# Kernel optimization log

Hardware: AMD Instinct MI355X
Metric: run time of the kernel (lower is better)

Reference implementation:

```python
import jax, jax.numpy as jnp
import numpy as np

B, T, E, H = 2, 2048, 1024, 16
D = E // H            # head dim = 64
ROT = D // 2          # rotary_dim = 32 (only first half of head dim is rotated)
THETA = 10000.0


def _rope(x):
    # x: (B, H, T, D). Faithful to rotary_embedding_torch.rotate_queries_or_keys
    # with dim=ROT: rotate first ROT features, interleaved-pair style, pass rest.
    t = x.shape[-2]
    inv = 1.0 / (THETA ** (jnp.arange(0, ROT, 2, dtype=jnp.float32) / ROT))   # (ROT//2,)
    freqs = jnp.arange(t, dtype=jnp.float32)[:, None] * inv[None, :]          # (T, ROT//2)
    freqs = jnp.repeat(freqs, 2, axis=-1)                                      # (T, ROT)
    cos, sin = jnp.cos(freqs), jnp.sin(freqs)
    xr, xp = x[..., :ROT], x[..., ROT:]
    p = xr.reshape(*xr.shape[:-1], ROT // 2, 2)
    rot = jnp.stack((-p[..., 1], p[..., 0]), axis=-1).reshape(xr.shape)
    return jnp.concatenate([xr * cos + rot * sin, xp], axis=-1)


def setup_inputs() -> dict:
    key = jax.random.key(0)
    k1, k2, k3 = jax.random.split(key, 3)
    query = jax.random.normal(k1, (B, T, E), dtype=jnp.float32)
    inputs = {
        "query": query,
        "key": query,            # ignored (cross_attention=False)
        "value": query,          # ignored
        "padding_mask": jnp.ones((B, T), dtype=bool),
        "in_proj_weight": jax.random.uniform(k2, (3 * E, E), dtype=jnp.float32),
        "out_proj_weight": jax.random.normal(k3, (E, E), dtype=jnp.float32) * (E ** -0.5),
    }
    return inputs


def reference(query, key, value, padding_mask, in_proj_weight, out_proj_weight):
    # cross_attention=False: key/value are overwritten by query
    key = query
    value = query
    q = query @ in_proj_weight[:E].T
    k = key @ in_proj_weight[E:2 * E].T
    v = value @ in_proj_weight[2 * E:].T
    # NOTE: raw reshape (B,T,E)->(B,H,T,D), exactly as in the torch module
    q = q.reshape(B, H, T, D)
    k = k.reshape(B, H, T, D)
    v = v.reshape(B, H, T, D)
    q = _rope(q)
    k = _rope(k)   # causal self-attention path: rotate keys too
    causal = jnp.tril(jnp.ones((T, T), dtype=bool))                 # (T, T)
    mask = causal[None, None] & padding_mask[:, None, None, :]      # (B,1,T,T) -> broadcast over H
    scores = jnp.einsum("bhqd,bhkd->bhqk", q, k) / jnp.sqrt(jnp.float32(D))
    scores = jnp.where(mask, scores, -jnp.inf)
    attn = jax.nn.softmax(scores, axis=-1)
    x = jnp.einsum("bhqk,bhkd->bhqd", attn, v)
    x = x.reshape(B, T, E)      # raw reshape back, as in torch
    return x @ out_proj_weight.T
```

## Files before the change

kernel.cpp:

```cpp
#include <hip/hip_runtime.h>
#include <stdint.h>

#define T_ 2048
#define E_ 1024

typedef __attribute__((ext_vector_type(8))) __bf16 bf16x8;
typedef __attribute__((ext_vector_type(4))) float f32x4;

__device__ __forceinline__ void gload_lds16(const void* g, void* l) {
  __builtin_amdgcn_global_load_lds(
      (const __attribute__((address_space(1))) unsigned int*)g,
      (__attribute__((address_space(3))) unsigned int*)l, 16, 0, 0);
}

__global__ __launch_bounds__(256) void k_split(const float4* __restrict__ src,
                                               ushort4* __restrict__ hi,
                                               ushort4* __restrict__ lo, int n4) {
  int i = blockIdx.x * 256 + threadIdx.x;
  if (i >= n4) return;
  float4 x = src[i];
  float xs[4] = {x.x, x.y, x.z, x.w};
  union { __bf16 b[4]; ushort4 u; } H, L;
#pragma unroll
  for (int j = 0; j < 4; ++j) {
    __bf16 h = (__bf16)xs[j];
    H.b[j] = h;
    L.b[j] = (__bf16)(xs[j] - (float)h);
  }
  hi[i] = H.u;
  lo[i] = L.u;
}

__global__ __launch_bounds__(256) void k_cvt(const float4* __restrict__ src,
                                             ushort4* __restrict__ dst, int n4) {
  int i = blockIdx.x * 256 + threadIdx.x;
  if (i >= n4) return;
  float4 x = src[i];
  float xs[4] = {x.x, x.y, x.z, x.w};
  union { __bf16 b[4]; ushort4 u; } H;
#pragma unroll
  for (int j = 0; j < 4; ++j) H.b[j] = (__bf16)xs[j];
  dst[i] = H.u;
}

__global__ __launch_bounds__(256) void k_table(float2* __restrict__ cs) {
  int i = blockIdx.x * 256 + threadIdx.x;
  int t = i >> 4, f = i & 15;
  double inv = pow(10000.0, -(double)f / 16.0);
  double ang = (double)t * inv;
  cs[i] = make_float2((float)cos(ang), (float)sin(ang));
}

template <int EPI, bool HILO>
__global__ __launch_bounds__(256) void k_gemm(const __bf16* __restrict__ Ah,
                                              const __bf16* __restrict__ Al,
                                              const __bf16* __restrict__ Bh,
                                              const __bf16* __restrict__ Bl,
                                              int M, int N, int K,
                                              const float2* __restrict__ cs,
                                              __bf16* __restrict__ qhi,
                                              __bf16* __restrict__ qlo,
                                              __bf16* __restrict__ khi,
                                              __bf16* __restrict__ klo,
                                              __bf16* __restrict__ v16,
                                              float* __restrict__ C32) {
  __shared__ __align__(16) __bf16 AsH[128 * 32];
  __shared__ __align__(16) __bf16 BsH[128 * 32];
  __shared__ __align__(16) __bf16 AsL[HILO ? 128 * 32 : 4];
  __shared__ __align__(16) __bf16 BsL[HILO ? 128 * 32 : 4];
  const int tid = threadIdx.x, lane = tid & 63, w = tid >> 6;
  const int wm = w >> 1, wn = w & 1;
  const int g = lane >> 4, d = lane & 15;
  const int m0 = blockIdx.y * 128, n0 = blockIdx.x * 128;

  f32x4 acc[4][4];
#pragma unroll
  for (int i = 0; i < 4; ++i)
#pragma unroll
    for (int j = 0; j < 4; ++j) acc[i][j] = (f32x4)(0.0f);

  const int row0 = tid >> 2, kc = tid & 3;
  const int row1 = 64 + row0;

  for (int k0 = 0; k0 < K; k0 += 32) {
    __syncthreads();
    gload_lds16(Ah + (size_t)(m0 + row0) * K + k0 + kc * 8, &AsH[w * 512]);
    gload_lds16(Ah + (size_t)(m0 + row1) * K + k0 + kc * 8, &AsH[2048 + w * 512]);
    gload_lds16(Bh + (size_t)(n0 + row0) * K + k0 + kc * 8, &BsH[w * 512]);
    gload_lds16(Bh + (size_t)(n0 + row1) * K + k0 + kc * 8, &BsH[2048 + w * 512]);
    if constexpr (HILO) {
      gload_lds16(Al + (size_t)(m0 + row0) * K + k0 + kc * 8, &AsL[w * 512]);
      gload_lds16(Al + (size_t)(m0 + row1) * K + k0 + kc * 8, &AsL[2048 + w * 512]);
      gload_lds16(Bl + (size_t)(n0 + row0) * K + k0 + kc * 8, &BsL[w * 512]);
      gload_lds16(Bl + (size_t)(n0 + row1) * K + k0 + kc * 8, &BsL[2048 + w * 512]);
    }
    __syncthreads();
    bf16x8 ah[4], bh[4], al[4], bl[4];
#pragma unroll
    for (int i = 0; i < 4; ++i) {
      ah[i] = *(const bf16x8*)&AsH[(wm * 64 + i * 16 + d) * 32 + g * 8];
      bh[i] = *(const bf16x8*)&BsH[(wn * 64 + i * 16 + d) * 32 + g * 8];
      if constexpr (HILO) {
        al[i] = *(const bf16x8*)&AsL[(wm * 64 + i * 16 + d) * 32 + g * 8];
        bl[i] = *(const bf16x8*)&BsL[(wn * 64 + i * 16 + d) * 32 + g * 8];
      }
    }
#pragma unroll
    for (int i = 0; i < 4; ++i)
#pragma unroll
      for (int j = 0; j < 4; ++j) {
        acc[i][j] = __builtin_amdgcn_mfma_f32_16x16x32_bf16(ah[i], bh[j], acc[i][j], 0, 0, 0);
        if constexpr (HILO) {
          acc[i][j] = __builtin_amdgcn_mfma_f32_16x16x32_bf16(al[i], bh[j], acc[i][j], 0, 0, 0);
          acc[i][j] = __builtin_amdgcn_mfma_f32_16x16x32_bf16(ah[i], bl[j], acc[i][j], 0, 0, 0);
        }
      }
  }

#pragma unroll
  for (int i = 0; i < 4; ++i) {
    const int rbase = m0 + wm * 64 + i * 16 + g * 4;
#pragma unroll
    for (int j = 0; j < 4; ++j) {
      const int col = n0 + wn * 64 + j * 16 + d;
#pragma unroll
      for (int r = 0; r < 4; ++r) {
        const float vv = acc[i][j][r];
        const int row = rbase + r;
        if constexpr (EPI == 0) {
          const float xp = __shfl_xor(vv, 1);
          const int which = col >> 10;
          const int cl = col & 1023;
          const int d2 = cl & 63;
          const int t2 = (row & 127) * 16 + (cl >> 6);
          float y;
          if (d2 < 32) {
            const float2 cse = cs[t2 * 16 + (d2 >> 1)];
            y = (d2 & 1) ? (vv * cse.x + xp * cse.y) : (vv * cse.x - xp * cse.y);
          } else {
            y = vv;
          }
          if (which == 0) y *= 0.18033688011112042f;
          const __bf16 hi = (__bf16)y;
          const __bf16 lo = (__bf16)(y - (float)hi);
          const size_t off = (size_t)row * 1024 + cl;
          (which ? khi : qhi)[off] = hi;
          (which ? klo : qlo)[off] = lo;
        } else if constexpr (EPI == 1) {
          C32[(size_t)row * N + col] = vv;
        } else {
          v16[(size_t)row * N + col] = (__bf16)vv;
        }
      }
    }
  }
}

__global__ __launch_bounds__(256) void k_vtrans(const __bf16* __restrict__ v16,
                                                __bf16* __restrict__ v16t) {
  __shared__ __bf16 TB[64][72];
  const int p = blockIdx.y, t0 = blockIdx.x * 64;
  const int tid = threadIdx.x;
  const int r = tid >> 2, c4 = (tid & 3) * 16;
  const __bf16* src = v16 + ((size_t)p * 2048 + t0 + r) * 64 + c4;
  bf16x8 A = *(const bf16x8*)src;
  bf16x8 B2 = *(const bf16x8*)(src + 8);
#pragma unroll
  for (int e = 0; e < 8; ++e) {
    TB[c4 + e][r] = A[e];
    TB[c4 + 8 + e][r] = B2[e];
  }
  __syncthreads();
  const int dd = tid >> 2, cc = (tid & 3) * 16;
  __bf16* dst = v16t + ((size_t)p * 64 + dd) * 2048 + t0 + cc;
  *(bf16x8*)dst = *(const bf16x8*)&TB[dd][cc];
  *(bf16x8*)(dst + 8) = *(const bf16x8*)&TB[dd][cc + 8];
}

__global__ __launch_bounds__(512, 4) void k_attn(const __bf16* __restrict__ qhi,
                                                 const __bf16* __restrict__ qlo,
                                                 const __bf16* __restrict__ khi,
                                                 const __bf16* __restrict__ klo,
                                                 const __bf16* __restrict__ v16t,
                                                 __bf16* __restrict__ x16,
                                                 float* __restrict__ po,
                                                 float* __restrict__ pm,
                                                 float* __restrict__ pl_) {
  __shared__ __align__(16) __bf16 KH[2][64 * 64];
  __shared__ __align__(16) __bf16 KL[2][64 * 64];
  __shared__ __align__(16) __bf16 VT[2][64 * 64];
  __shared__ __align__(16) __bf16 PL[8][16 * 72];

  const int b = blockIdx.x, panel = blockIdx.y;
  const int u0 = 9 * b;
  int qtA = 0;
  while (2 * (qtA + 1) * (qtA + 2) <= u0) ++qtA;
  const int cumA = 2 * qtA * (qtA + 1);
  const int cumB = 2 * (qtA + 1) * (qtA + 2);
  const int jloA = u0 - cumA;
  const bool two = (u0 + 9 > cumB);
  const int jhiA = two ? (cumB - 1 - cumA) : (u0 + 8 - cumA);
  const int jhiB = u0 + 8 - cumB;

  const int tid = threadIdx.x, lane = tid & 63, w = tid >> 6;
  const int g = lane >> 4, d = lane & 15;
  const size_t hb = (size_t)panel * T_ * 64;

  const int kr = tid >> 3, kc = tid & 7;
  const int swz = (kc ^ (kr & 7)) * 8;
  const __bf16* kB = khi + hb;
  const __bf16* lB = klo + hb;
  const __bf16* vB = v16t + (size_t)panel * (64 * T_);

#define STAGE(j, bb)                                                        \
  {                                                                         \
    gload_lds16(kB + (size_t)((j) * 64 + kr) * 64 + swz, &KH[bb][w * 512]); \
    gload_lds16(lB + (size_t)((j) * 64 + kr) * 64 + swz, &KL[bb][w * 512]); \
    gload_lds16(vB + (size_t)kr * T_ + (j) * 64 + swz, &VT[bb][w * 512]);   \
  }

  int cur = 0;
  STAGE(jloA, 0);

  for (int seg = 0; seg < 2; ++seg) {
    if (seg && !two) break;
    const int qt = qtA + seg;
    const int jlo = seg ? 0 : jloA;
    const int jhi = seg ? jhiB : jhiA;
    const int q0 = qt << 8;

    bf16x8 qh[2][2], ql[2][2];
#pragma unroll
    for (int rb = 0; rb < 2; ++rb) {
      const int rbi = w * 2 + rb;
      const size_t qrow = hb + (size_t)(q0 + rbi * 16 + d) * 64;
      qh[rb][0] = *(const bf16x8*)&qhi[qrow + g * 8];
      qh[rb][1] = *(const bf16x8*)&qhi[qrow + 32 + g * 8];
      ql[rb][0] = *(const bf16x8*)&qlo[qrow + g * 8];
      ql[rb][1] = *(const bf16x8*)&qlo[qrow + 32 + g * 8];
    }

    f32x4 o[2][4];
#pragma unroll
    for (int rb = 0; rb < 2; ++rb)
#pragma unroll
      for (int i = 0; i < 4; ++i) o[rb][i] = (f32x4)(0.0f);
    float m_[2] = {-__builtin_inff(), -__builtin_inff()};
    float l_[2] = {0.0f, 0.0f};

    for (int j = jlo; j <= jhi; ++j) {
      __syncthreads();
      if (j < jhi) {
        STAGE(j + 1, cur ^ 1);
      } else if (!seg && two) {
        STAGE(0, cur ^ 1);
      }

#pragma unroll
      for (int rb = 0; rb < 2; ++rb) {
        const int rbi = w * 2 + rb;
        const int qrow0 = q0 + rbi * 16;
        if (j * 64 > qrow0 + 15) continue;

        f32x4 s[4];
        __builtin_amdgcn_s_setprio(1);
#pragma unroll
        for (int f = 0; f < 4; ++f) {
          f32x4 accs = (f32x4)(0.0f);
          const int colr = f * 16 + d;
#pragma unroll
          for (int ds = 0; ds < 2; ++ds) {
            const int slot = ((ds * 4 + g) ^ (colr & 7)) * 8;
            const bf16x8 kf = *(const bf16x8*)&KH[cur][colr * 64 + slot];
            const bf16x8 lf = *(const bf16x8*)&KL[cur][colr * 64 + slot];
            accs = __builtin_amdgcn_mfma_f32_16x16x32_bf16(kf, qh[rb][ds], accs, 0, 0, 0);
            accs = __builtin_amdgcn_mfma_f32_16x16x32_bf16(kf, ql[rb][ds], accs, 0, 0, 0);
            accs = __builtin_amdgcn_mfma_f32_16x16x32_bf16(lf, qh[rb][ds], accs, 0, 0, 0);
          }
          s[f] = accs;
        }
        __builtin_amdgcn_s_setprio(0);

        if (j * 64 + 63 > qrow0) {
          const int qq = qrow0 + d;
#pragma unroll
          for (int f = 0; f < 4; ++f)
#pragma unroll
            for (int r = 0; r < 4; ++r) {
              const int kv = j * 64 + f * 16 + g * 4 + r;
              if (kv > qq) s[f][r] = -30000.0f;
            }
        }

        float pmax = fmaxf(fmaxf(s[0][0], s[0][1]), fmaxf(s[0][2], s[0][3]));
#pragma unroll
        for (int f = 1; f < 4; ++f)
          pmax = fmaxf(pmax, fmaxf(fmaxf(s[f][0], s[f][1]), fmaxf(s[f][2], s[f][3])));
        pmax = fmaxf(pmax, __shfl_xor(pmax, 16));
        pmax = fmaxf(pmax, __shfl_xor(pmax, 32));

        if (!__all(pmax - m_[rb] <= 11.5f)) {
          const float mnew = fmaxf(m_[rb], pmax);
          const float fac = exp2f(m_[rb] - mnew);
          m_[rb] = mnew;
          float facr[4];
#pragma unroll
          for (int r = 0; r < 4; ++r)
            facr[r] = __shfl(fac, (lane & 48) | (g * 4 + r));
#pragma unroll
          for (int ni = 0; ni < 4; ++ni)
#pragma unroll
            for (int r = 0; r < 4; ++r) o[rb][ni][r] *= facr[r];
          l_[rb] *= fac;
        }

        float sum = 0.0f;
#pragma unroll
        for (int f = 0; f < 4; ++f) {
          union { __bf16 b[4]; ushort4 u4; } pk;
#pragma unroll
          for (int r = 0; r < 4; ++r) {
            const float pv = exp2f(s[f][r] - m_[rb]);
            sum += pv;
            pk.b[r] = (__bf16)pv;
          }
          *(ushort4*)&PL[w][d * 72 + f * 16 + g * 4] = pk.u4;
        }
        sum += __shfl_xor(sum, 16);
        sum += __shfl_xor(sum, 32);
        l_[rb] += sum;

        __builtin_amdgcn_s_setprio(1);
#pragma unroll
        for (int ks = 0; ks < 2; ++ks) {
          const bf16x8 pa = *(const bf16x8*)&PL[w][d * 72 + ks * 32 + g * 8];
#pragma unroll
          for (int ni = 0; ni < 4; ++ni) {
            const bf16x8 vf =
                *(const bf16x8*)&VT[cur][(ni * 16 + d) * 64 + (((ks * 4 + g) ^ (d & 7)) * 8)];
            o[rb][ni] = __builtin_amdgcn_mfma_f32_16x16x32_bf16(pa, vf, o[rb][ni], 0, 0, 0);
          }
        }
        __builtin_amdgcn_s_setprio(0);
      }
      cur ^= 1;
    }

    const int slot = panel * 23 + b + qt;
#pragma unroll
    for (int rb = 0; rb < 2; ++rb) {
      const int rbi = w * 2 + rb;
#pragma unroll
      for (int ni = 0; ni < 4; ++ni)
#pragma unroll
        for (int r = 0; r < 4; ++r) {
          const int rowin = rbi * 16 + g * 4 + r;
          po[(size_t)slot * 16384 + rowin * 64 + ni * 16 + d] = o[rb][ni][r];
        }
      if (g == 0) {
        pm[slot * 256 + rbi * 16 + d] = m_[rb];
        pl_[slot * 256 + rbi * 16 + d] = l_[rb];
      }
    }
  }
#undef STAGE
}

__global__ __launch_bounds__(256) void k_combine(const float* __restrict__ po,
                                                 const float* __restrict__ pm,
                                                 const float* __restrict__ pl_,
                                                 __bf16* __restrict__ x16) {
  const int p = blockIdx.y;
  const int li = blockIdx.x * 256 + threadIdx.x;
  const int d = li & 63;
  const int t2 = li >> 6;
  const int qt = t2 >> 8;
  const int rowin = t2 & 255;
  const int cq = 2 * qt * (qt + 1);
  const int nc = (cq + 4 * qt + 3) / 9 - cq / 9 + 1;
  const int s0 = p * 23 + cq / 9 + qt;
  float M = -__builtin_inff();
  for (int s = 0; s < nc; ++s) M = fmaxf(M, pm[(s0 + s) * 256 + rowin]);
  float L = 0.0f, O = 0.0f;
  for (int s = 0; s < nc; ++s) {
    const float ww = exp2f(pm[(s0 + s) * 256 + rowin] - M);
    L += pl_[(s0 + s) * 256 + rowin] * ww;
    O += po[(size_t)(s0 + s) * 16384 + rowin * 64 + d] * ww;
  }
  x16[((size_t)p * T_ + t2) * 64 + d] = (__bf16)(O / L);
}

extern "C" void kernel_launch(void* const* d_in, const int* in_sizes, int n_in,
                              void* d_out, int out_size, void* d_ws, size_t ws_size,
                              hipStream_t stream) {
  const float* query = (const float*)d_in[0];
  const float* win = (const float*)d_in[4];
  const float* wout = (const float*)d_in[5];
  float* out = (float*)d_out;

  const size_t MB = 1024 * 1024;
  const size_t KB = 1024;
  char* ws = (char*)d_ws;
  __bf16* xh = (__bf16*)(ws);
  __bf16* xl = (__bf16*)(ws + 8 * MB);
  __bf16* whh = (__bf16*)(ws + 16 * MB);
  __bf16* whl = (__bf16*)(ws + 22 * MB);
  __bf16* wob = (__bf16*)(ws + 28 * MB);
  float* pm = (float*)(ws + 30 * MB);
  float* pl_ = (float*)(ws + 30 * MB + 768 * KB);
  float2* cs = (float2*)(ws + 31 * MB + 512 * KB);
  float* po = (float*)(ws + 32 * MB);
  __bf16* qhi = (__bf16*)(ws + 78 * MB);
  __bf16* qlo = (__bf16*)(ws + 86 * MB);
  __bf16* khi = (__bf16*)(ws + 94 * MB);
  __bf16* klo = (__bf16*)(ws + 102 * MB);
  __bf16* x16 = (__bf16*)(ws + 78 * MB);
  __bf16* v16 = (__bf16*)(ws + 64 * MB);
  __bf16* v16t = (__bf16*)(ws);

  k_split<<<4096, 256, 0, stream>>>((const float4*)query, (ushort4*)xh, (ushort4*)xl,
                                    4096 * 1024 / 4);
  k_split<<<3072, 256, 0, stream>>>((const float4*)win, (ushort4*)whh, (ushort4*)whl,
                                    3072 * 1024 / 4);
  k_cvt<<<1024, 256, 0, stream>>>((const float4*)wout, (ushort4*)wob, 1024 * 1024 / 4);
  k_table<<<128, 256, 0, stream>>>(cs);

  dim3 gqk(16, 32);
  k_gemm<0, true><<<gqk, 256, 0, stream>>>(xh, xl, whh, whl, 4096, 2048, 1024, cs,
                                           qhi, qlo, khi, klo, nullptr, nullptr);
  dim3 gv(8, 32);
  k_gemm<2, false><<<gv, 256, 0, stream>>>(xh, nullptr, whh + (size_t)2048 * 1024, nullptr,
                                           4096, 1024, 1024, nullptr, nullptr, nullptr,
                                           nullptr, nullptr, v16, nullptr);

  dim3 gt(32, 32);
  k_vtrans<<<gt, 256, 0, stream>>>(v16, v16t);

  dim3 ga(16, 32);
  k_attn<<<ga, 512, 0, stream>>>(qhi, qlo, khi, klo, v16t, x16, po, pm, pl_);

  dim3 gc(512, 32);
  k_combine<<<gc, 256, 0, stream>>>(po, pm, pl_, x16);

  dim3 go(8, 32);
  k_gemm<1, false><<<go, 256, 0, stream>>>(x16, nullptr, wob, nullptr, 4096, 1024, 1024,
                                           nullptr, nullptr, nullptr, nullptr, nullptr,
                                           nullptr, out);
}
```

Before: 217.0 us.

## Fuse prep kernels, use 64-row GEMM tiles, rebalance attention work by cost

Merges the four preprocessing kernels (split, convert, RoPE table) into one launch to cut launch overhead. Adds a 64x128-tile GEMM for the V projection and output projection, doubling block count on the plain bf16 GEMMs so more CUs are occupied. Changes attention work partitioning from equal tile counts to a cost-weighted split where diagonal tiles weigh less, with the combine kernel's slot indexing updated to match. The risk is a mismatch between the attention split and the combine indexing, plus lower per-block reuse in the smaller GEMM tiles.

After: 211.7 us. -2.5%, faster.

```diff
diff --git a/kernel.cpp b/kernel.cpp
--- a/kernel.cpp
+++ b/kernel.cpp
@@ -13,42 +13,48 @@
       (__attribute__((address_space(3))) unsigned int*)l, 16, 0, 0);
 }
 
-__global__ __launch_bounds__(256) void k_split(const float4* __restrict__ src,
-                                               ushort4* __restrict__ hi,
-                                               ushort4* __restrict__ lo, int n4) {
-  int i = blockIdx.x * 256 + threadIdx.x;
-  if (i >= n4) return;
-  float4 x = src[i];
-  float xs[4] = {x.x, x.y, x.z, x.w};
-  union { __bf16 b[4]; ushort4 u; } H, L;
-#pragma unroll
-  for (int j = 0; j < 4; ++j) {
-    __bf16 h = (__bf16)xs[j];
-    H.b[j] = h;
-    L.b[j] = (__bf16)(xs[j] - (float)h);
-  }
-  hi[i] = H.u;
-  lo[i] = L.u;
-}
-
-__global__ __launch_bounds__(256) void k_cvt(const float4* __restrict__ src,
-                                             ushort4* __restrict__ dst, int n4) {
-  int i = blockIdx.x * 256 + threadIdx.x;
-  if (i >= n4) return;
-  float4 x = src[i];
-  float xs[4] = {x.x, x.y, x.z, x.w};
-  union { __bf16 b[4]; ushort4 u; } H;
-#pragma unroll
-  for (int j = 0; j < 4; ++j) H.b[j] = (__bf16)xs[j];
-  dst[i] = H.u;
-}
-
-__global__ __launch_bounds__(256) void k_table(float2* __restrict__ cs) {
-  int i = blockIdx.x * 256 + threadIdx.x;
-  int t = i >> 4, f = i & 15;
-  double inv = pow(10000.0, -(double)f / 16.0);
-  double ang = (double)t * inv;
-  cs[i] = make_float2((float)cos(ang), (float)sin(ang));
+__global__ __launch_bounds__(256) void k_prep(const float4* __restrict__ q,
+                                              ushort4* __restrict__ xh,
+                                              ushort4* __restrict__ xl,
+                                              const float4* __restrict__ win,
+                                              ushort4* __restrict__ whh,
+                                              ushort4* __restrict__ whl,
+                                              const float4* __restrict__ wout,
+                                              ushort4* __restrict__ wob,
+                                              float2* __restrict__ cs) {
+  const int b = blockIdx.x, tid = threadIdx.x;
+  if (b < 7168) {
+    const float4* src;
+    ushort4 *hi, *lo;
+    int i;
+    if (b < 4096) { src = q; hi = xh; lo = xl; i = b * 256 + tid; }
+    else          { src = win; hi = whh; lo = whl; i = (b - 4096) * 256 + tid; }
+    float4 x = src[i];
+    float xs[4] = {x.x, x.y, x.z, x.w};
+    union { __bf16 bb[4]; ushort4 u; } H, L;
+#pragma unroll
+    for (int jj = 0; jj < 4; ++jj) {
+      __bf16 h = (__bf16)xs[jj];
+      H.bb[jj] = h;
+      L.bb[jj] = (__bf16)(xs[jj] - (float)h);
+    }
+    hi[i] = H.u;
+    lo[i] = L.u;
+  } else if (b < 8192) {
+    int i = (b - 7168) * 256 + tid;
+    float4 x = wout[i];
+    float xs[4] = {x.x, x.y, x.z, x.w};
+    union { __bf16 bb[4]; ushort4 u; } H;
+#pragma unroll
+    for (int jj = 0; jj < 4; ++jj) H.bb[jj] = (__bf16)xs[jj];
+    wob[i] = H.u;
+  } else {
+    int i = (b - 8192) * 256 + tid;
+    int t = i >> 4, f = i & 15;
+    double inv = pow(10000.0, -(double)f / 16.0);
+    double ang = (double)t * inv;
+    cs[i] = make_float2((float)cos(ang), (float)sin(ang));
+  }
 }
 
 template <int EPI, bool HILO>
@@ -156,6 +162,62 @@
   }
 }
 
+template <int EPI>
+__global__ __launch_bounds__(256) void k_gemm64(const __bf16* __restrict__ Ah,
+                                                const __bf16* __restrict__ Bh,
+                                                int M, int N, int K,
+                                                __bf16* __restrict__ v16,
+                                                float* __restrict__ C32) {
+  __shared__ __align__(16) __bf16 As[64 * 32];
+  __shared__ __align__(16) __bf16 Bs[128 * 32];
+  const int tid = threadIdx.x, lane = tid & 63, w = tid >> 6;
+  const int g = lane >> 4, d = lane & 15;
+  const int m0 = blockIdx.y * 64, n0 = blockIdx.x * 128;
+
+  f32x4 acc[4][2];
+#pragma unroll
+  for (int i = 0; i < 4; ++i)
+#pragma unroll
+    for (int j = 0; j < 2; ++j) acc[i][j] = (f32x4)(0.0f);
+
+  const int row0 = tid >> 2, kc = tid & 3;
+  const int row1 = 64 + row0;
+
+  for (int k0 = 0; k0 < K; k0 += 32) {
+    __syncthreads();
+    gload_lds16(Ah + (size_t)(m0 + row0) * K + k0 + kc * 8, &As[w * 512]);
+    gload_lds16(Bh + (size_t)(n0 + row0) * K + k0 + kc * 8, &Bs[w * 512]);
+    gload_lds16(Bh + (size_t)(n0 + row1) * K + k0 + kc * 8, &Bs[2048 + w * 512]);
+    __syncthreads();
+    bf16x8 ah[4], bh[2];
+#pragma unroll
+    for (int i = 0; i < 4; ++i) ah[i] = *(const bf16x8*)&As[(i * 16 + d) * 32 + g * 8];
+#pragma unroll
+    for (int j = 0; j < 2; ++j)
+      bh[j] = *(const bf16x8*)&Bs[(w * 32 + j * 16 + d) * 32 + g * 8];
+#pragma unroll
+    for (int i = 0; i < 4; ++i)
+#pragma unroll
+      for (int j = 0; j < 2; ++j)
+        acc[i][j] = __builtin_amdgcn_mfma_f32_16x16x32_bf16(ah[i], bh[j], acc[i][j], 0, 0, 0);
+  }
+
+#pragma unroll
+  for (int i = 0; i < 4; ++i) {
+    const int rbase = m0 + i * 16 + g * 4;
+#pragma unroll
+    for (int j = 0; j < 2; ++j) {
+      const int col = n0 + w * 32 + j * 16 + d;
+#pragma unroll
+      for (int r = 0; r < 4; ++r) {
+        const int row = rbase + r;
+        if constexpr (EPI == 1) C32[(size_t)row * N + col] = acc[i][j][r];
+        else v16[(size_t)row * N + col] = (__bf16)acc[i][j][r];
+      }
+    }
+  }
+}
+
 __global__ __launch_bounds__(256) void k_vtrans(const __bf16* __restrict__ v16,
                                                 __bf16* __restrict__ v16t) {
   __shared__ __bf16 TB[64][72];
@@ -175,6 +237,20 @@
   __bf16* dst = v16t + ((size_t)p * 64 + dd) * 2048 + t0 + cc;
   *(bf16x8*)dst = *(const bf16x8*)&TB[dd][cc];
   *(bf16x8*)(dst + 8) = *(const bf16x8*)&TB[dd][cc + 8];
+}
+
+__device__ __forceinline__ void find_unit(int W, int& qt, int& j) {
+  qt = 0;
+#pragma unroll
+  for (int q = 1; q <= 7; ++q)
+    if (40 * q * q + 16 * q <= W) qt = q;
+  int s = 40 * qt * qt + 16 * qt;
+  j = 0;
+  while (s < W) {
+    int p = j - 4 * qt;
+    s += (p < 0) ? 20 : 20 - 4 * p;
+    ++j;
+  }
 }
 
 __global__ __launch_bounds__(512, 4) void k_attn(const __bf16* __restrict__ qhi,
@@ -192,15 +268,13 @@
   __shared__ __align__(16) __bf16 PL[8][16 * 72];
 
   const int b = blockIdx.x, panel = blockIdx.y;
-  const int u0 = 9 * b;
-  int qtA = 0;
-  while (2 * (qtA + 1) * (qtA + 2) <= u0) ++qtA;
-  const int cumA = 2 * qtA * (qtA + 1);
-  const int cumB = 2 * (qtA + 1) * (qtA + 2);
-  const int jloA = u0 - cumA;
-  const bool two = (u0 + 9 > cumB);
-  const int jhiA = two ? (cumB - 1 - cumA) : (u0 + 8 - cumA);
-  const int jhiB = u0 + 8 - cumB;
+  int qtA, jA, qtE, jE;
+  find_unit(168 * b, qtA, jA);
+  find_unit(168 * (b + 1), qtE, jE);
+  int nseg, jhi0, jhi1 = 0;
+  if (qtE == qtA)      { nseg = 1; jhi0 = jE - 1; }
+  else if (jE == 0)    { nseg = 1; jhi0 = 4 * qtA + 3; }
+  else                 { nseg = 2; jhi0 = 4 * qtA + 3; jhi1 = jE - 1; }
 
   const int tid = threadIdx.x, lane = tid & 63, w = tid >> 6;
   const int g = lane >> 4, d = lane & 15;
@@ -220,13 +294,14 @@
   }
 
   int cur = 0;
-  STAGE(jloA, 0);
-
+  STAGE(jA, 0);
+
+#pragma unroll
   for (int seg = 0; seg < 2; ++seg) {
-    if (seg && !two) break;
+    if (seg >= nseg) break;
     const int qt = qtA + seg;
-    const int jlo = seg ? 0 : jloA;
-    const int jhi = seg ? jhiB : jhiA;
+    const int jlo = seg ? 0 : jA;
+    const int jhi = seg ? jhi1 : jhi0;
     const int q0 = qt << 8;
 
     bf16x8 qh[2][2], ql[2][2];
@@ -252,7 +327,7 @@
       __syncthreads();
       if (j < jhi) {
         STAGE(j + 1, cur ^ 1);
-      } else if (!seg && two) {
+      } else if (!seg && nseg == 2) {
         STAGE(0, cur ^ 1);
       }
 
@@ -317,12 +392,12 @@
         float sum = 0.0f;
 #pragma unroll
         for (int f = 0; f < 4; ++f) {
-          union { __bf16 b[4]; ushort4 u4; } pk;
+          union { __bf16 bb[4]; ushort4 u4; } pk;
 #pragma unroll
           for (int r = 0; r < 4; ++r) {
             const float pv = exp2f(s[f][r] - m_[rb]);
             sum += pv;
-            pk.b[r] = (__bf16)pv;
+            pk.bb[r] = (__bf16)pv;
           }
           *(ushort4*)&PL[w][d * 72 + f * 16 + g * 4] = pk.u4;
         }
@@ -376,9 +451,9 @@
   const int t2 = li >> 6;
   const int qt = t2 >> 8;
   const int rowin = t2 & 255;
-  const int cq = 2 * qt * (qt + 1);
-  const int nc = (cq + 4 * qt + 3) / 9 - cq / 9 + 1;
-  const int s0 = p * 23 + cq / 9 + qt;
+  const int cq = 40 * qt * qt + 16 * qt;
+  const int nc = (cq + 80 * qt + 48) / 168 - cq / 168 + 1;
+  const int s0 = p * 23 + cq / 168 + qt;
   float M = -__builtin_inff();
   for (int s = 0; s < nc; ++s) M = fmaxf(M, pm[(s0 + s) * 256 + rowin]);
   float L = 0.0f, O = 0.0f;
@@ -418,20 +493,16 @@
   __bf16* v16 = (__bf16*)(ws + 64 * MB);
   __bf16* v16t = (__bf16*)(ws);
 
-  k_split<<<4096, 256, 0, stream>>>((const float4*)query, (ushort4*)xh, (ushort4*)xl,
-                                    4096 * 1024 / 4);
-  k_split<<<3072, 256, 0, stream>>>((const float4*)win, (ushort4*)whh, (ushort4*)whl,
-                                    3072 * 1024 / 4);
-  k_cvt<<<1024, 256, 0, stream>>>((const float4*)wout, (ushort4*)wob, 1024 * 1024 / 4);
-  k_table<<<128, 256, 0, stream>>>(cs);
+  k_prep<<<8320, 256, 0, stream>>>((const float4*)query, (ushort4*)xh, (ushort4*)xl,
+                                   (const float4*)win, (ushort4*)whh, (ushort4*)whl,
+                                   (const float4*)wout, (ushort4*)wob, cs);
 
   dim3 gqk(16, 32);
   k_gemm<0, true><<<gqk, 256, 0, stream>>>(xh, xl, whh, whl, 4096, 2048, 1024, cs,
                                            qhi, qlo, khi, klo, nullptr, nullptr);
-  dim3 gv(8, 32);
-  k_gemm<2, false><<<gv, 256, 0, stream>>>(xh, nullptr, whh + (size_t)2048 * 1024, nullptr,
-                                           4096, 1024, 1024, nullptr, nullptr, nullptr,
-                                           nullptr, nullptr, v16, nullptr);
+  dim3 gv(8, 64);
+  k_gemm64<2><<<gv, 256, 0, stream>>>(xh, whh + (size_t)2048 * 1024, 4096, 1024, 1024,
+                                      v16, nullptr);
 
   dim3 gt(32, 32);
   k_vtrans<<<gt, 256, 0, stream>>>(v16, v16t);
@@ -442,8 +513,6 @@
   dim3 gc(512, 32);
   k_combine<<<gc, 256, 0, stream>>>(po, pm, pl_, x16);
 
-  dim3 go(8, 32);
-  k_gemm<1, false><<<go, 256, 0, stream>>>(x16, nullptr, wob, nullptr, 4096, 1024, 1024,
-                                           nullptr, nullptr, nullptr, nullptr, nullptr,
-                                           nullptr, out);
-}
+  dim3 go(8, 64);
+  k_gemm64<1><<<go, 256, 0, stream>>>(x16, wob, 4096, 1024, 1024, nullptr, out);
+}
```
